# Kernel optimization log

Hardware: AMD Instinct MI355X
Metric: run time of the kernel (lower is better)

The kernel has to match this reference:

```python
import jax, jax.numpy as jnp
import numpy as np

B, CIN, COUT, K, H, W, STYLE_DIM = 16, 128, 128, 3, 128, 128, 512

def setup_inputs() -> dict:
    key = jax.random.key(0)
    k1, k2, k3, k4 = jax.random.split(key, 4)
    x = jax.random.normal(k1, (B, CIN, H, W), dtype=jnp.float32)
    style = jax.random.normal(k2, (B, STYLE_DIM), dtype=jnp.float32)
    weight = jax.random.normal(k3, (COUT, CIN, K, K), dtype=jnp.float32)
    mod_w = jax.random.normal(k4, (CIN, STYLE_DIM), dtype=jnp.float32)
    mod_b = jnp.ones((CIN,), dtype=jnp.float32)  # EqualLinear bias_init=1
    return {"x": x, "style": style, "weight": weight, "mod_w": mod_w, "mod_b": mod_b}

def reference(x, style, weight, mod_w, mod_b):
    b, cin, h, w = x.shape
    cout, _, k, _ = weight.shape
    scale = 1.0 / np.sqrt(cin * k * k)        # conv equalized-lr scale
    lin_scale = 1.0 / np.sqrt(mod_w.shape[1])  # EqualLinear scale (lr_mul=1)
    pad = k // 2
    # affine modulation: EqualLinear(style_dim -> in_channels), bias_init=1
    s = style @ (mod_w * lin_scale).T + mod_b               # [B, Cin]
    # per-sample modulated weights
    wmod = scale * weight[None] * s[:, None, :, None, None]  # [B, Cout, Cin, k, k]
    demod = jax.lax.rsqrt(jnp.sum(wmod * wmod, axis=(2, 3, 4)) + 1e-8)  # [B, Cout]
    wmod = wmod * demod[:, :, None, None, None]
    # grouped conv with groups=batch == vmapped per-sample conv
    def conv_one(xi, wi):
        return jax.lax.conv_general_dilated(
            xi[None], wi, window_strides=(1, 1), padding=[(pad, pad), (pad, pad)],
            dimension_numbers=("NCHW", "OIHW", "NCHW"))[0]
    out = jax.vmap(conv_one)(x, wmod)  # [B, Cout, H, W]
    return out
```

## Files before the change

### kernel.cpp

```cpp
#include <hip/hip_runtime.h>
#include <hip/hip_bf16.h>


typedef __attribute__((ext_vector_type(8))) short short8;
typedef __attribute__((ext_vector_type(4))) float f32x4;

#define CONV_SCALE 0.029462782549439483f
#define LIN_SCALE 0.04419417382415922f

__device__ __forceinline__ void async16(unsigned short* lds, const unsigned short* g) {
  __builtin_amdgcn_global_load_lds((const __attribute__((address_space(1))) void*)g,
                                   (__attribute__((address_space(3))) void*)lds, 16, 0, 0);
}

__device__ __forceinline__ unsigned int pack2bf(float a, float b) {
  unsigned short ha = __builtin_bit_cast(unsigned short, __float2bfloat16(a));
  unsigned short hb = __builtin_bit_cast(unsigned short, __float2bfloat16(b));
  return (unsigned int)ha | ((unsigned int)hb << 16);
}

__global__ void style_kernel(const float* __restrict__ style, const float* __restrict__ mod_w,
                             const float* __restrict__ mod_b, float* __restrict__ s_ws) {
  const int gw = blockIdx.x * 4 + (threadIdx.x >> 6);
  const int b = gw >> 7, cin = gw & 127, lane = threadIdx.x & 63;
  const float4 s0 = *(const float4*)(style + (size_t)b * 512 + lane * 4);
  const float4 s1 = *(const float4*)(style + (size_t)b * 512 + 256 + lane * 4);
  const float4 w0 = *(const float4*)(mod_w + (size_t)cin * 512 + lane * 4);
  const float4 w1 = *(const float4*)(mod_w + (size_t)cin * 512 + 256 + lane * 4);
  float acc = s0.x * w0.x + s0.y * w0.y + s0.z * w0.z + s0.w * w0.w +
              s1.x * w1.x + s1.y * w1.y + s1.z * w1.z + s1.w * w1.w;
#pragma unroll
  for (int off = 32; off; off >>= 1) acc += __shfl_xor(acc, off);
  if (lane == 0) s_ws[b * 128 + cin] = acc * LIN_SCALE + mod_b[cin];
}

__global__ void modw_kernel(const float* __restrict__ weight, const float* __restrict__ s_ws,
                            unsigned short* __restrict__ w_ws) {
  const int bid = blockIdx.x;
  const int b = bid >> 7, cout = bid & 127;
  const int cin = threadIdx.x;
  const float sv = s_ws[b * 128 + cin] * CONV_SCALE;
  const float* wp = weight + ((size_t)cout * 128 + cin) * 9;
  float v[9];
  float ss = 0.f;
#pragma unroll
  for (int j = 0; j < 9; ++j) { v[j] = wp[j] * sv; ss += v[j] * v[j]; }
#pragma unroll
  for (int off = 32; off; off >>= 1) ss += __shfl_down(ss, off);
  __shared__ float red[2];
  if ((threadIdx.x & 63) == 0) red[threadIdx.x >> 6] = ss;
  __syncthreads();
  const float dem = rsqrtf(red[0] + red[1] + 1e-8f);
#pragma unroll
  for (int j = 0; j < 9; ++j) {
    __hip_bfloat16 h = __float2bfloat16(v[j] * dem);
    w_ws[(((size_t)b * 9 + j) * 128 + cout) * 128 + cin] =
        __builtin_bit_cast(unsigned short, h);
  }
}

__global__ __launch_bounds__(256, 2) void conv_kernel(const float* __restrict__ x,
                                                      const unsigned short* __restrict__ wws,
                                                      float* __restrict__ out) {
  __shared__ unsigned short xr[3 * 128 * 64];
  __shared__ unsigned short lA[128 * 64];

  const int tid = threadIdx.x;
  const int bid = (blockIdx.x & 7) * 256 + (blockIdx.x >> 3);
  const int b = bid >> 7, y = bid & 127;
  const int lane = tid & 63, w = tid >> 6;
  const int wm = w & 1, wn = w >> 1;
  const int l15 = lane & 15, q = lane >> 4;

  f32x4 acc[4][4];
#pragma unroll
  for (int i = 0; i < 4; ++i)
#pragma unroll
    for (int t = 0; t < 4; ++t) acc[i][t] = (f32x4){0.f, 0.f, 0.f, 0.f};

  const float* xb = x + (size_t)b * (128 * 16384);
  const unsigned short* wb = wws + (size_t)b * 9 * 128 * 128;

  const int mbase = tid >> 3;
  const int goff = (((tid & 7) ^ ((tid >> 3) & 7)) << 3);
  const int eoff = tid * 8;

  const int xq = tid & 31, cq8 = tid >> 5;
  const int tg16 = tid & 7, txr = tid >> 3;

  int nt[4];
#pragma unroll
  for (int t = 0; t < 4; ++t) nt[t] = wn * 64 + t * 16 + l15;

  const short8 zero8 = {0, 0, 0, 0, 0, 0, 0, 0};

  for (int c0 = 0; c0 < 128; c0 += 64) {
#pragma unroll
    for (int r3 = 0; r3 < 3; ++r3) {
      const int yy = y + r3 - 1;
      if (yy < 0 || yy > 127) continue;
      __syncthreads();
      const float* xrow = xb + (size_t)c0 * 16384 + (size_t)yy * 128;
      float4 f[2][4];
#pragma unroll
      for (int rr = 0; rr < 2; ++rr)
#pragma unroll
        for (int j = 0; j < 4; ++j)
          f[rr][j] = *(const float4*)(xrow + (size_t)(rr * 32 + cq8 * 4 + j) * 16384 + xq * 4);
#pragma unroll
      for (int rr = 0; rr < 2; ++rr) {
        const int g8 = rr * 8 + cq8;
#pragma unroll
        for (int i = 0; i < 4; ++i) {
          const int xp = xq * 4 + i;
          const int gp = g8 ^ (xp & 15);
          uint2 col;
          col.x = pack2bf(((const float*)&f[rr][0])[i], ((const float*)&f[rr][1])[i]);
          col.y = pack2bf(((const float*)&f[rr][2])[i], ((const float*)&f[rr][3])[i]);
          *(uint2*)(lA + xp * 64 + gp * 4) = col;
        }
      }
      __syncthreads();
#pragma unroll
      for (int rr = 0; rr < 4; ++rr) {
        const int xp = rr * 32 + txr;
        const int s15 = xp & 15;
        const int gp0 = (tg16 * 2) ^ s15, gp1 = (tg16 * 2 + 1) ^ s15;
        const uint2 a = *(const uint2*)(lA + xp * 64 + gp0 * 4);
        const uint2 c = *(const uint2*)(lA + xp * 64 + gp1 * 4);
        uint4 o;
        o.x = a.x; o.y = a.y; o.z = c.x; o.w = c.y;
        *(uint4*)(xr + r3 * 8192 + xp * 64 + ((tg16 ^ (xp & 7)) << 3)) = o;
      }
    }

    for (int j3 = 0; j3 < 9; ++j3) {
      const int ky = j3 / 3, kx = j3 - ky * 3;
      const int yy = y + ky - 1;
      if (yy < 0 || yy > 127) continue;
      __syncthreads();
#pragma unroll
      for (int p = 0; p < 4; ++p)
        async16(lA + p * 2048 + eoff, wb + j3 * 16384 + c0 + p * 4096 + mbase * 128 + goff);
      int xcb[4];
#pragma unroll
      for (int t = 0; t < 4; ++t) xcb[t] = nt[t] + (kx - 1);
      const bool lo = (xcb[0] < 0);
      const bool hi = (xcb[3] > 127);
      if (lo) xcb[0] = 0;
      if (hi) xcb[3] = 127;
      const unsigned short* xkr = xr + ky * 8192;
      __syncthreads();
#pragma unroll
      for (int s = 0; s < 2; ++s) {
        const int s4q = s * 4 + q;
        const int axor = ((s4q ^ (l15 & 7)) << 3);
        short8 af[4], bf[4];
#pragma unroll
        for (int i = 0; i < 4; ++i)
          af[i] = *(const short8*)(lA + (wm * 64 + i * 16 + l15) * 64 + axor);
#pragma unroll
        for (int t = 0; t < 4; ++t)
          bf[t] = *(const short8*)(xkr + xcb[t] * 64 + ((s4q ^ (xcb[t] & 7)) << 3));
        if (lo) bf[0] = zero8;
        if (hi) bf[3] = zero8;
#pragma unroll
        for (int i = 0; i < 4; ++i)
#pragma unroll
          for (int t = 0; t < 4; ++t)
            acc[i][t] = __builtin_amdgcn_mfma_f32_16x16x32_bf16(af[i], bf[t], acc[i][t], 0, 0, 0);
      }
    }
  }

  float* ob = out + ((size_t)b * 128 * 128 + y) * 128;
#pragma unroll
  for (int i = 0; i < 4; ++i) {
    const int coutb = wm * 64 + i * 16 + q * 4;
#pragma unroll
    for (int r = 0; r < 4; ++r) {
      float* orow = ob + (size_t)(coutb + r) * (128 * 128);
#pragma unroll
      for (int t = 0; t < 4; ++t) orow[wn * 64 + t * 16 + l15] = acc[i][t][r];
    }
  }
}

extern "C" void kernel_launch(void* const* d_in, const int* in_sizes, int n_in,
                              void* d_out, int out_size, void* d_ws, size_t ws_size,
                              hipStream_t stream) {
  const float* x = (const float*)d_in[0];
  const float* style = (const float*)d_in[1];
  const float* weight = (const float*)d_in[2];
  const float* mod_w = (const float*)d_in[3];
  const float* mod_b = (const float*)d_in[4];
  float* out = (float*)d_out;

  char* ws = (char*)d_ws;
  float* s_ws = (float*)ws;
  unsigned short* w_ws = (unsigned short*)(ws + 8192);

  style_kernel<<<512, 256, 0, stream>>>(style, mod_w, mod_b, s_ws);
  modw_kernel<<<16 * 128, 128, 0, stream>>>(weight, s_ws, w_ws);
  conv_kernel<<<16 * 128, 256, 0, stream>>>(x, w_ws, out);
}
```

Before: 307.3 us.

## Compute two output rows per block, sharing weight tiles across a rolling row buffer

Each block now handles two adjacent output rows with 512 threads. Each modulated-weight tile loaded into LDS serves both rows, so weight traffic per output row is halved. Input rows are held in a two-slot rolling buffer that loads one new row per ky step, and padding rows are zero-filled instead of skipped. The transpose now writes straight into the swizzled layout without the old staging pass through lA. In exchange the block is larger with more barriers per step, and boundary rows now run full MFMA work on zeros.

```diff
diff --git a/kernel.cpp b/kernel.cpp
--- a/kernel.cpp
+++ b/kernel.cpp
@@ -59,17 +59,44 @@
   }
 }
 
-__global__ __launch_bounds__(256, 2) void conv_kernel(const float* __restrict__ x,
+__device__ __forceinline__ void transpose_row(const float* __restrict__ xb, int c0, int yy,
+                                              unsigned short* __restrict__ dst, int tid) {
+  const int tcq = tid & 15, txq = tid >> 4;
+  if (yy < 0 || yy > 127) {
+    const uint2 z = {0u, 0u};
+#pragma unroll
+    for (int i = 0; i < 4; ++i) {
+      const int xp = txq * 4 + i;
+      *(uint2*)(dst + xp * 64 + (((tcq >> 1) ^ (xp & 7)) << 3) + ((tcq & 1) << 2)) = z;
+    }
+    return;
+  }
+  const float* row = xb + (size_t)(c0 + tcq * 4) * 16384 + (size_t)yy * 128 + txq * 4;
+  float4 f[4];
+#pragma unroll
+  for (int j = 0; j < 4; ++j) f[j] = *(const float4*)(row + (size_t)j * 16384);
+#pragma unroll
+  for (int i = 0; i < 4; ++i) {
+    const int xp = txq * 4 + i;
+    uint2 col;
+    col.x = pack2bf(((const float*)&f[0])[i], ((const float*)&f[1])[i]);
+    col.y = pack2bf(((const float*)&f[2])[i], ((const float*)&f[3])[i]);
+    *(uint2*)(dst + xp * 64 + (((tcq >> 1) ^ (xp & 7)) << 3) + ((tcq & 1) << 2)) = col;
+  }
+}
+
+__global__ __launch_bounds__(512, 4) void conv_kernel(const float* __restrict__ x,
                                                       const unsigned short* __restrict__ wws,
                                                       float* __restrict__ out) {
-  __shared__ unsigned short xr[3 * 128 * 64];
+  __shared__ unsigned short xr[2 * 128 * 64];
   __shared__ unsigned short lA[128 * 64];
 
   const int tid = threadIdx.x;
-  const int bid = (blockIdx.x & 7) * 256 + (blockIdx.x >> 3);
-  const int b = bid >> 7, y = bid & 127;
+  const int bid = (blockIdx.x & 7) * 128 + (blockIdx.x >> 3);
+  const int b = bid >> 6, y0 = (bid & 63) * 2;
   const int lane = tid & 63, w = tid >> 6;
   const int wm = w & 1, wn = w >> 1;
+  const int r = wn >> 1, xh = wn & 1;
   const int l15 = lane & 15, q = lane >> 4;
 
   f32x4 acc[4][4];
@@ -81,107 +108,69 @@
   const float* xb = x + (size_t)b * (128 * 16384);
   const unsigned short* wb = wws + (size_t)b * 9 * 128 * 128;
 
-  const int mbase = tid >> 3;
   const int goff = (((tid & 7) ^ ((tid >> 3) & 7)) << 3);
+  const int m0 = tid >> 3;
   const int eoff = tid * 8;
-
-  const int xq = tid & 31, cq8 = tid >> 5;
-  const int tg16 = tid & 7, txr = tid >> 3;
 
   int nt[4];
 #pragma unroll
-  for (int t = 0; t < 4; ++t) nt[t] = wn * 64 + t * 16 + l15;
+  for (int t = 0; t < 4; ++t) nt[t] = xh * 64 + t * 16 + l15;
 
   const short8 zero8 = {0, 0, 0, 0, 0, 0, 0, 0};
 
   for (int c0 = 0; c0 < 128; c0 += 64) {
+    __syncthreads();
+    transpose_row(xb, c0, y0 - 1, xr, tid);
+    transpose_row(xb, c0, y0, xr + 8192, tid);
+    for (int ky = 0; ky < 3; ++ky) {
+      for (int kx = 0; kx < 3; ++kx) {
+        const int j3 = ky * 3 + kx;
+        if (j3) __syncthreads();
+        async16(lA + eoff, wb + j3 * 16384 + c0 + m0 * 128 + goff);
+        async16(lA + 4096 + eoff, wb + j3 * 16384 + c0 + (64 + m0) * 128 + goff);
+        if (kx == 0 && ky > 0)
+          transpose_row(xb, c0, y0 + ky, xr + (((ky + 1) & 1) << 13), tid);
+        __syncthreads();
+        const unsigned short* xkr = xr + (((ky + r) & 1) << 13);
+        int xcb[4];
 #pragma unroll
-    for (int r3 = 0; r3 < 3; ++r3) {
-      const int yy = y + r3 - 1;
-      if (yy < 0 || yy > 127) continue;
-      __syncthreads();
-      const float* xrow = xb + (size_t)c0 * 16384 + (size_t)yy * 128;
-      float4 f[2][4];
+        for (int t = 0; t < 4; ++t) xcb[t] = nt[t] + (kx - 1);
+        const bool lo = (xcb[0] < 0);
+        const bool hi = (xcb[3] > 127);
+        if (lo) xcb[0] = 0;
+        if (hi) xcb[3] = 127;
 #pragma unroll
-      for (int rr = 0; rr < 2; ++rr)
+        for (int s = 0; s < 2; ++s) {
+          const int s4q = s * 4 + q;
+          const int axor = ((s4q ^ (l15 & 7)) << 3);
+          short8 af[4], bf[4];
 #pragma unroll
-        for (int j = 0; j < 4; ++j)
-          f[rr][j] = *(const float4*)(xrow + (size_t)(rr * 32 + cq8 * 4 + j) * 16384 + xq * 4);
-#pragma unroll
-      for (int rr = 0; rr < 2; ++rr) {
-        const int g8 = rr * 8 + cq8;
-#pragma unroll
-        for (int i = 0; i < 4; ++i) {
-          const int xp = xq * 4 + i;
-          const int gp = g8 ^ (xp & 15);
-          uint2 col;
-          col.x = pack2bf(((const float*)&f[rr][0])[i], ((const float*)&f[rr][1])[i]);
-          col.y = pack2bf(((const float*)&f[rr][2])[i], ((const float*)&f[rr][3])[i]);
-          *(uint2*)(lA + xp * 64 + gp * 4) = col;
-        }
-      }
-      __syncthreads();
-#pragma unroll
-      for (int rr = 0; rr < 4; ++rr) {
-        const int xp = rr * 32 + txr;
-        const int s15 = xp & 15;
-        const int gp0 = (tg16 * 2) ^ s15, gp1 = (tg16 * 2 + 1) ^ s15;
-        const uint2 a = *(const uint2*)(lA + xp * 64 + gp0 * 4);
-        const uint2 c = *(const uint2*)(lA + xp * 64 + gp1 * 4);
-        uint4 o;
-        o.x = a.x; o.y = a.y; o.z = c.x; o.w = c.y;
-        *(uint4*)(xr + r3 * 8192 + xp * 64 + ((tg16 ^ (xp & 7)) << 3)) = o;
-      }
-    }
-
-    for (int j3 = 0; j3 < 9; ++j3) {
-      const int ky = j3 / 3, kx = j3 - ky * 3;
-      const int yy = y + ky - 1;
-      if (yy < 0 || yy > 127) continue;
-      __syncthreads();
-#pragma unroll
-      for (int p = 0; p < 4; ++p)
-        async16(lA + p * 2048 + eoff, wb + j3 * 16384 + c0 + p * 4096 + mbase * 128 + goff);
-      int xcb[4];
-#pragma unroll
-      for (int t = 0; t < 4; ++t) xcb[t] = nt[t] + (kx - 1);
-      const bool lo = (xcb[0] < 0);
-      const bool hi = (xcb[3] > 127);
-      if (lo) xcb[0] = 0;
-      if (hi) xcb[3] = 127;
-      const unsigned short* xkr = xr + ky * 8192;
-      __syncthreads();
-#pragma unroll
-      for (int s = 0; s < 2; ++s) {
-        const int s4q = s * 4 + q;
-        const int axor = ((s4q ^ (l15 & 7)) << 3);
-        short8 af[4], bf[4];
-#pragma unroll
-        for (int i = 0; i < 4; ++i)
-          af[i] = *(const short8*)(lA + (wm * 64 + i * 16 + l15) * 64 + axor);
-#pragma unroll
-        for (int t = 0; t < 4; ++t)
-          bf[t] = *(const short8*)(xkr + xcb[t] * 64 + ((s4q ^ (xcb[t] & 7)) << 3));
-        if (lo) bf[0] = zero8;
-        if (hi) bf[3] = zero8;
-#pragma unroll
-        for (int i = 0; i < 4; ++i)
+          for (int i = 0; i < 4; ++i)
+            af[i] = *(const short8*)(lA + (wm * 64 + i * 16 + l15) * 64 + axor);
 #pragma unroll
           for (int t = 0; t < 4; ++t)
-            acc[i][t] = __builtin_amdgcn_mfma_f32_16x16x32_bf16(af[i], bf[t], acc[i][t], 0, 0, 0);
+            bf[t] = *(const short8*)(xkr + xcb[t] * 64 + ((s4q ^ (xcb[t] & 7)) << 3));
+          if (lo) bf[0] = zero8;
+          if (hi) bf[3] = zero8;
+#pragma unroll
+          for (int i = 0; i < 4; ++i)
+#pragma unroll
+            for (int t = 0; t < 4; ++t)
+              acc[i][t] = __builtin_amdgcn_mfma_f32_16x16x32_bf16(af[i], bf[t], acc[i][t], 0, 0, 0);
+        }
       }
     }
   }
 
-  float* ob = out + ((size_t)b * 128 * 128 + y) * 128;
+  float* ob = out + ((size_t)b * 128 * 128 + (y0 + r)) * 128;
 #pragma unroll
   for (int i = 0; i < 4; ++i) {
     const int coutb = wm * 64 + i * 16 + q * 4;
 #pragma unroll
-    for (int r = 0; r < 4; ++r) {
-      float* orow = ob + (size_t)(coutb + r) * (128 * 128);
+    for (int rr = 0; rr < 4; ++rr) {
+      float* orow = ob + (size_t)(coutb + rr) * (128 * 128);
 #pragma unroll
-      for (int t = 0; t < 4; ++t) orow[wn * 64 + t * 16 + l15] = acc[i][t][r];
+      for (int t = 0; t < 4; ++t) orow[xh * 64 + t * 16 + l15] = acc[i][t][rr];
     }
   }
 }
@@ -202,5 +191,5 @@
 
   style_kernel<<<512, 256, 0, stream>>>(style, mod_w, mod_b, s_ws);
   modw_kernel<<<16 * 128, 128, 0, stream>>>(weight, s_ws, w_ws);
-  conv_kernel<<<16 * 128, 256, 0, stream>>>(x, w_ws, out);
+  conv_kernel<<<16 * 64, 512, 0, stream>>>(x, w_ws, out);
 }
```

Result: slower. 385.4 us (+25.4%).
